# Performance work log

Hardware: AMD Instinct MI355X
Metric: run time of the kernel (lower is better)

The kernel has to match this reference:

```python
import jax, jax.numpy as jnp
import numpy as np

BIT_SHIFT = 8
H, W = 480, 640
N = 100000
C_IN, C_HID, C_OUT = 96, 576, 96


def setup_inputs() -> dict:
    key = jax.random.key(0)
    ks = jax.random.split(key, 12)
    # --- sparse 2D coordinates (unique active sites on an H x W grid) ---
    rng = np.random.default_rng(0)
    lin = rng.choice(H * W, size=N, replace=False)
    ys, xs = lin // W, lin % W
    grid = -np.ones((H, W), dtype=np.int32)
    grid[ys, xs] = np.arange(N, dtype=np.int32)
    # neighbor index for each of the 9 kernel offsets; -1 where no active neighbor
    nbr = np.empty((9, N), dtype=np.int32)
    k = 0
    for dy in (-1, 0, 1):
        for dx in (-1, 0, 1):
            yn, xn = ys + dy, xs + dx
            valid = (yn >= 0) & (yn < H) & (xn >= 0) & (xn < W)
            idx = grid[np.clip(yn, 0, H - 1), np.clip(xn, 0, W - 1)]
            nbr[k] = np.where(valid, idx, -1)
            k += 1
    # --- int8-valued float features / weights (quantized integer inference) ---
    feats = jnp.round(jnp.clip(30.0 * jax.random.normal(ks[0], (N, C_IN)), -127, 127))
    w1 = jnp.round(jnp.clip(40.0 * jax.random.normal(ks[1], (C_IN, C_HID)), -127, 127))
    b1 = jnp.round(1000.0 * jax.random.normal(ks[2], (C_HID,)))
    w2 = jnp.round(jnp.clip(40.0 * jax.random.normal(ks[3], (9, C_HID)), -127, 127))
    b2 = jnp.round(1000.0 * jax.random.normal(ks[4], (C_HID,)))
    w3 = jnp.round(jnp.clip(40.0 * jax.random.normal(ks[5], (C_HID, C_OUT)), -127, 127))
    b3 = jnp.round(1000.0 * jax.random.normal(ks[6], (C_OUT,)))
    # per-output-channel requantization scaling factors (>= ~1 so round() is nonzero)
    s1 = 1.0 + 3.0 * jax.random.uniform(ks[7], (C_HID,))
    s2 = 1.0 + 3.0 * jax.random.uniform(ks[8], (C_HID,))
    s3 = 1.0 + 3.0 * jax.random.uniform(ks[9], (C_OUT,))
    s_main = 1.0 + 2.0 * jax.random.uniform(ks[10], ())
    s_res = 1.0 + 2.0 * jax.random.uniform(ks[11], ())
    return {"feats": feats, "neighbor_idx": jnp.asarray(nbr), "w1": w1, "b1": b1,
            "w2": w2, "b2": b2, "w3": w3, "b3": b3,
            "s1": s1, "s2": s2, "s3": s3, "s_main": s_main, "s_res": s_res}


def _requant(acc, s):
    # fused integer rescale: multiplier m = round(s) * 2^bit_shift, then /2^(2*bit_shift)
    B = 2.0 ** BIT_SHIFT
    return acc * (jnp.round(s) * B) / (B * B)


def _clamp(x):
    lim = 2.0 ** (BIT_SHIFT - 1)
    return jnp.clip(x, -lim, lim)


def _relu6(x):
    return jnp.clip(x, 0.0, 6.0)


def reference(feats, neighbor_idx, w1, b1, w2, b2, w3, b3, s1, s2, s3, s_main, s_res):
    B = 2.0 ** BIT_SHIFT
    # 1x1 expand conv (dense GEMM over active sites)
    x = _relu6(_clamp(_requant(feats @ w1 + b1, s1)))  # [N, C_HID]
    # depthwise 3x3 sparse conv: gather 9 neighbor taps, mask missing sites
    mask = (neighbor_idx >= 0).astype(x.dtype)               # [9, N]
    gathered = x[jnp.clip(neighbor_idx, 0, None)] * mask[:, :, None]  # [9, N, C_HID]
    dw = jnp.einsum('knc,kc->nc', gathered, w2) + b2
    x = _relu6(_clamp(_requant(dw, s2)))
    # 1x1 project conv
    x = _clamp(_requant(x @ w3 + b3, s3))                    # [N, C_OUT]
    # scaled residual add
    out = jnp.round(s_main) * B * x + jnp.round(s_res) * B * feats
    return out
```

## Files before the change

kernel.cpp:

```cpp
#include <hip/hip_runtime.h>
#include <hip/hip_bf16.h>
#include <hip/hip_fp16.h>

#define NS   100000
#define CIN  96
#define CHID 576
#define COUT 96
#define SPB  32
#define LDH  (CHID + 8)
#define CPT  8
#define NG   (CHID / CPT)
#define NSLOT (576 / NG)
#define SPS  (SPB / NSLOT)

typedef float    floatx4 __attribute__((ext_vector_type(4)));
typedef int      intx4   __attribute__((ext_vector_type(4)));
typedef short    short8  __attribute__((ext_vector_type(8)));
typedef _Float16 half8   __attribute__((ext_vector_type(8)));
typedef _Float16 half4   __attribute__((ext_vector_type(4)));

__global__ void prep_kernel(const float* __restrict__ w1, const float* __restrict__ w3,
                            const float* __restrict__ w2,
                            unsigned short* __restrict__ w1T, _Float16* __restrict__ w3T,
                            _Float16* __restrict__ w2h, _Float16* __restrict__ x1h) {
  int i = blockIdx.x * blockDim.x + threadIdx.x;
  if (i >= CHID * CIN) return;
  if (i < CHID) x1h[(size_t)NS * CHID + i] = (_Float16)0.0f;
  if (i < 9 * CHID) w2h[i] = (_Float16)w2[i];
  {
    int h = i / CIN, k = i % CIN;
    w1T[i] = (unsigned short)(__float_as_uint(w1[k * CHID + h]) >> 16);
  }
  {
    int o = i / CHID, k = i % CHID;
    w3T[i] = (_Float16)w3[k * COUT + o];
  }
}

__global__ __launch_bounds__(64) void expand_kernel(
    const float* __restrict__ feats, const float* __restrict__ b1,
    const float* __restrict__ s1, const unsigned short* __restrict__ w1T,
    _Float16* __restrict__ x1h) {
  const int lane = threadIdx.x;
  const int m = lane & 15, quad = lane >> 4;
  const int s0 = blockIdx.x * 64;

  short8 bfrag[4][3];
#pragma unroll
  for (int u = 0; u < 4; ++u) {
    const int site = min(s0 + u * 16 + m, NS - 1);
    const float* frow = feats + (size_t)site * CIN + quad * 8;
#pragma unroll
    for (int kc = 0; kc < 3; ++kc) {
      const float4 lo = *reinterpret_cast<const float4*>(frow + kc * 32);
      const float4 hi = *reinterpret_cast<const float4*>(frow + kc * 32 + 4);
      const float v[8] = {lo.x, lo.y, lo.z, lo.w, hi.x, hi.y, hi.z, hi.w};
#pragma unroll
      for (int j = 0; j < 8; ++j)
        bfrag[u][kc][j] = (short)(__float_as_uint(v[j]) >> 16);
    }
  }

  const int hq = quad * 4;
#pragma unroll 2
  for (int ht = 0; ht < CHID / 16; ++ht) {
    const unsigned short* wrow = w1T + (ht * 16 + m) * CIN + quad * 8;
    short8 a[3];
#pragma unroll
    for (int kc = 0; kc < 3; ++kc)
      a[kc] = *reinterpret_cast<const short8*>(wrow + kc * 32);

    floatx4 acc[4] = {{0.f, 0.f, 0.f, 0.f}, {0.f, 0.f, 0.f, 0.f},
                      {0.f, 0.f, 0.f, 0.f}, {0.f, 0.f, 0.f, 0.f}};
#pragma unroll
    for (int kc = 0; kc < 3; ++kc)
#pragma unroll
      for (int u = 0; u < 4; ++u)
        acc[u] = __builtin_amdgcn_mfma_f32_16x16x32_bf16(a[kc], bfrag[u][kc], acc[u], 0, 0, 0);

    const floatx4 bv = *reinterpret_cast<const floatx4*>(b1 + ht * 16 + hq);
    const floatx4 sv = *reinterpret_cast<const floatx4*>(s1 + ht * 16 + hq);
    floatx4 sc;
#pragma unroll
    for (int j = 0; j < 4; ++j) sc[j] = rintf(sv[j]) * (1.0f / 256.0f);

#pragma unroll
    for (int u = 0; u < 4; ++u) {
      const int site = s0 + u * 16 + m;
      if (site < NS) {
        half4 r;
#pragma unroll
        for (int j = 0; j < 4; ++j) {
          float v = (acc[u][j] + bv[j]) * sc[j];
          r[j] = (_Float16)fminf(fmaxf(v, 0.0f), 6.0f);
        }
        *reinterpret_cast<half4*>(x1h + (size_t)site * CHID + ht * 16 + hq) = r;
      }
    }
  }
}

__global__ __launch_bounds__(576, 8) void dwproj_kernel(
    const int* __restrict__ nbr, const _Float16* __restrict__ w2h,
    const float* __restrict__ b2, const float* __restrict__ s2,
    const _Float16* __restrict__ x1h, const _Float16* __restrict__ w3T,
    const float* __restrict__ feats, const float* __restrict__ b3,
    const float* __restrict__ s3, const float* __restrict__ s_main,
    const float* __restrict__ s_res, float* __restrict__ out) {
  __shared__ _Float16 x2t[SPB * LDH];
  __shared__ int offt[SPB * 12];
  const int t = threadIdx.x;
  const int s0 = blockIdx.x * SPB;

  if (t < SPB * 9) {
    const int k = t >> 5, n = t & 31;
    const int idx = nbr[k * NS + s0 + n];
    offt[n * 12 + k] = (idx < 0 ? NS : idx) * CHID;
  }
  __syncthreads();

  {
    const int g = t % NG;
    const int slot = t / NG;
    const int c0 = g * CPT;
    half8 wv[9];
#pragma unroll
    for (int k = 0; k < 9; ++k)
      wv[k] = *reinterpret_cast<const half8*>(w2h + k * CHID + c0);

#pragma unroll
    for (int i = 0; i < SPS; ++i) {
      const int n = slot * SPS + i;
      const intx4 oa = *reinterpret_cast<const intx4*>(offt + n * 12);
      const intx4 ob = *reinterpret_cast<const intx4*>(offt + n * 12 + 4);
      const int o8 = offt[n * 12 + 8];
      half8 v0 = *reinterpret_cast<const half8*>(x1h + (size_t)oa.x + c0);
      half8 v1 = *reinterpret_cast<const half8*>(x1h + (size_t)oa.y + c0);
      half8 v2 = *reinterpret_cast<const half8*>(x1h + (size_t)oa.z + c0);
      half8 v3 = *reinterpret_cast<const half8*>(x1h + (size_t)oa.w + c0);
      half8 v4 = *reinterpret_cast<const half8*>(x1h + (size_t)ob.x + c0);
      half8 v5 = *reinterpret_cast<const half8*>(x1h + (size_t)ob.y + c0);
      half8 v6 = *reinterpret_cast<const half8*>(x1h + (size_t)ob.z + c0);
      half8 v7 = *reinterpret_cast<const half8*>(x1h + (size_t)ob.w + c0);
      half8 v8 = *reinterpret_cast<const half8*>(x1h + (size_t)o8 + c0);
      float acc[8];
      {
        const floatx4 b0 = *reinterpret_cast<const floatx4*>(b2 + c0);
        const floatx4 b1v = *reinterpret_cast<const floatx4*>(b2 + c0 + 4);
#pragma unroll
        for (int j = 0; j < 4; ++j) { acc[j] = b0[j]; acc[j + 4] = b1v[j]; }
      }
#pragma unroll
      for (int j = 0; j < 8; ++j) {
        acc[j] += (float)v0[j] * (float)wv[0][j];
        acc[j] += (float)v1[j] * (float)wv[1][j];
        acc[j] += (float)v2[j] * (float)wv[2][j];
        acc[j] += (float)v3[j] * (float)wv[3][j];
        acc[j] += (float)v4[j] * (float)wv[4][j];
        acc[j] += (float)v5[j] * (float)wv[5][j];
        acc[j] += (float)v6[j] * (float)wv[6][j];
        acc[j] += (float)v7[j] * (float)wv[7][j];
        acc[j] += (float)v8[j] * (float)wv[8][j];
      }
      const floatx4 sa = *reinterpret_cast<const floatx4*>(s2 + c0);
      const floatx4 sb = *reinterpret_cast<const floatx4*>(s2 + c0 + 4);
      half8 r;
#pragma unroll
      for (int j = 0; j < 4; ++j) {
        float va = acc[j]     * (rintf(sa[j]) * (1.0f / 256.0f));
        float vb = acc[j + 4] * (rintf(sb[j]) * (1.0f / 256.0f));
        r[j]     = (_Float16)fminf(fmaxf(va, 0.0f), 6.0f);
        r[j + 4] = (_Float16)fminf(fmaxf(vb, 0.0f), 6.0f);
      }
      *reinterpret_cast<half8*>(x2t + n * LDH + c0) = r;
    }
  }
  __syncthreads();

  const int wave = t >> 6, lane = t & 63;
  const int m = lane & 15, quad = lane >> 4;
  const float rsm = rintf(s_main[0]) * 256.0f;
  const float rsr = rintf(s_res[0]) * 256.0f;

  for (int tile = wave; tile < (SPB / 16) * (COUT / 16); tile += 9) {
    const int tm = tile / (COUT / 16);
    const int ot = tile % (COUT / 16);
    floatx4 acc = {0.f, 0.f, 0.f, 0.f};
    const _Float16* arow = w3T + (ot * 16 + m) * CHID + quad * 8;
    const _Float16* blds = x2t + (tm * 16 + m) * LDH + quad * 8;
#pragma unroll
    for (int kc = 0; kc < 18; ++kc) {
      const half8 a = *reinterpret_cast<const half8*>(arow + kc * 32);
      const half8 b = *reinterpret_cast<const half8*>(blds + kc * 32);
      acc = __builtin_amdgcn_mfma_f32_16x16x32_f16(a, b, acc, 0, 0, 0);
    }
    const int site = s0 + tm * 16 + m;
    const int o0 = ot * 16 + quad * 4;
    const floatx4 b3v = *reinterpret_cast<const floatx4*>(b3 + o0);
    const floatx4 s3v = *reinterpret_cast<const floatx4*>(s3 + o0);
    const floatx4 fv =
        *reinterpret_cast<const floatx4*>(feats + (size_t)site * COUT + o0);
    floatx4 r;
#pragma unroll
    for (int j = 0; j < 4; ++j) {
      float v = (acc[j] + b3v[j]) * (rintf(s3v[j]) * (1.0f / 256.0f));
      v = fminf(fmaxf(v, -128.0f), 128.0f);
      r[j] = rsm * v + rsr * fv[j];
    }
    *reinterpret_cast<floatx4*>(out + (size_t)site * COUT + o0) = r;
  }
}

extern "C" void kernel_launch(void* const* d_in, const int* in_sizes, int n_in,
                              void* d_out, int out_size, void* d_ws, size_t ws_size,
                              hipStream_t stream) {
  const float* feats  = (const float*)d_in[0];
  const int*   nbr    = (const int*)d_in[1];
  const float* w1     = (const float*)d_in[2];
  const float* b1     = (const float*)d_in[3];
  const float* w2     = (const float*)d_in[4];
  const float* b2     = (const float*)d_in[5];
  const float* w3     = (const float*)d_in[6];
  const float* b3     = (const float*)d_in[7];
  const float* s1     = (const float*)d_in[8];
  const float* s2     = (const float*)d_in[9];
  const float* s3     = (const float*)d_in[10];
  const float* s_main = (const float*)d_in[11];
  const float* s_res  = (const float*)d_in[12];
  float* out = (float*)d_out;

  char* ws = (char*)d_ws;
  _Float16*       x1h = (_Float16*)ws;
  unsigned short* w1T = (unsigned short*)(ws + 115201152);
  _Float16*       w3T = (_Float16*)(ws + 115311744);
  _Float16*       w2h = (_Float16*)(ws + 115422336);

  prep_kernel<<<(CHID * CIN + 255) / 256, 256, 0, stream>>>(w1, w3, w2, w1T, w3T, w2h, x1h);
  expand_kernel<<<(NS + 63) / 64, 64, 0, stream>>>(feats, b1, s1, w1T, x1h);
  dwproj_kernel<<<NS / SPB, 576, 0, stream>>>(nbr, w2h, b2, s2, x1h, w3T,
                                              feats, b3, s3, s_main, s_res, out);
}
```

Measured before the change: 342.9 us.

## Split expand across four waves and shrink dwproj blocks to 256 threads

The expand kernel now launches 256 threads per block, with each of the four waves computing 9 of the 36 hidden-channel tiles for the same 64 sites. This gives four times more waves in flight and less serial work per wave. The dwproj kernel drops from 576 to 256 threads and walks the 32x72 (site, channel-group) work items in 9 strided iterations. Depthwise weights are now reloaded every iteration instead of held in registers, and the projection MFMA tiles are spread over 4 waves instead of 9. The aim is better occupancy and latency hiding, at the cost of redundant feature loads in expand and more serial projection work per wave.

```diff
diff --git a/kernel.cpp b/kernel.cpp
--- a/kernel.cpp
+++ b/kernel.cpp
@@ -8,10 +8,6 @@
 #define COUT 96
 #define SPB  32
 #define LDH  (CHID + 8)
-#define CPT  8
-#define NG   (CHID / CPT)
-#define NSLOT (576 / NG)
-#define SPS  (SPB / NSLOT)
 
 typedef float    floatx4 __attribute__((ext_vector_type(4)));
 typedef int      intx4   __attribute__((ext_vector_type(4)));
@@ -37,11 +33,12 @@
   }
 }
 
-__global__ __launch_bounds__(64) void expand_kernel(
+__global__ __launch_bounds__(256, 4) void expand_kernel(
     const float* __restrict__ feats, const float* __restrict__ b1,
     const float* __restrict__ s1, const unsigned short* __restrict__ w1T,
     _Float16* __restrict__ x1h) {
-  const int lane = threadIdx.x;
+  const int t = threadIdx.x;
+  const int wave = t >> 6, lane = t & 63;
   const int m = lane & 15, quad = lane >> 4;
   const int s0 = blockIdx.x * 64;
 
@@ -62,8 +59,9 @@
   }
 
   const int hq = quad * 4;
-#pragma unroll 2
-  for (int ht = 0; ht < CHID / 16; ++ht) {
+  const int ht0 = wave * 9;
+#pragma unroll 3
+  for (int ht = ht0; ht < ht0 + 9; ++ht) {
     const unsigned short* wrow = w1T + (ht * 16 + m) * CIN + quad * 8;
     short8 a[3];
 #pragma unroll
@@ -100,7 +98,7 @@
   }
 }
 
-__global__ __launch_bounds__(576, 8) void dwproj_kernel(
+__global__ __launch_bounds__(256, 4) void dwproj_kernel(
     const int* __restrict__ nbr, const _Float16* __restrict__ w2h,
     const float* __restrict__ b2, const float* __restrict__ s2,
     const _Float16* __restrict__ x1h, const _Float16* __restrict__ w3T,
@@ -112,68 +110,70 @@
   const int t = threadIdx.x;
   const int s0 = blockIdx.x * SPB;
 
-  if (t < SPB * 9) {
-    const int k = t >> 5, n = t & 31;
+  for (int i = t; i < SPB * 9; i += 256) {
+    const int k = i >> 5, n = i & 31;
     const int idx = nbr[k * NS + s0 + n];
     offt[n * 12 + k] = (idx < 0 ? NS : idx) * CHID;
   }
   __syncthreads();
 
-  {
-    const int g = t % NG;
-    const int slot = t / NG;
-    const int c0 = g * CPT;
-    half8 wv[9];
-#pragma unroll
-    for (int k = 0; k < 9; ++k)
-      wv[k] = *reinterpret_cast<const half8*>(w2h + k * CHID + c0);
-
-#pragma unroll
-    for (int i = 0; i < SPS; ++i) {
-      const int n = slot * SPS + i;
-      const intx4 oa = *reinterpret_cast<const intx4*>(offt + n * 12);
-      const intx4 ob = *reinterpret_cast<const intx4*>(offt + n * 12 + 4);
-      const int o8 = offt[n * 12 + 8];
-      half8 v0 = *reinterpret_cast<const half8*>(x1h + (size_t)oa.x + c0);
-      half8 v1 = *reinterpret_cast<const half8*>(x1h + (size_t)oa.y + c0);
-      half8 v2 = *reinterpret_cast<const half8*>(x1h + (size_t)oa.z + c0);
-      half8 v3 = *reinterpret_cast<const half8*>(x1h + (size_t)oa.w + c0);
-      half8 v4 = *reinterpret_cast<const half8*>(x1h + (size_t)ob.x + c0);
-      half8 v5 = *reinterpret_cast<const half8*>(x1h + (size_t)ob.y + c0);
-      half8 v6 = *reinterpret_cast<const half8*>(x1h + (size_t)ob.z + c0);
-      half8 v7 = *reinterpret_cast<const half8*>(x1h + (size_t)ob.w + c0);
-      half8 v8 = *reinterpret_cast<const half8*>(x1h + (size_t)o8 + c0);
-      float acc[8];
-      {
-        const floatx4 b0 = *reinterpret_cast<const floatx4*>(b2 + c0);
-        const floatx4 b1v = *reinterpret_cast<const floatx4*>(b2 + c0 + 4);
-#pragma unroll
-        for (int j = 0; j < 4; ++j) { acc[j] = b0[j]; acc[j + 4] = b1v[j]; }
-      }
-#pragma unroll
-      for (int j = 0; j < 8; ++j) {
-        acc[j] += (float)v0[j] * (float)wv[0][j];
-        acc[j] += (float)v1[j] * (float)wv[1][j];
-        acc[j] += (float)v2[j] * (float)wv[2][j];
-        acc[j] += (float)v3[j] * (float)wv[3][j];
-        acc[j] += (float)v4[j] * (float)wv[4][j];
-        acc[j] += (float)v5[j] * (float)wv[5][j];
-        acc[j] += (float)v6[j] * (float)wv[6][j];
-        acc[j] += (float)v7[j] * (float)wv[7][j];
-        acc[j] += (float)v8[j] * (float)wv[8][j];
-      }
-      const floatx4 sa = *reinterpret_cast<const floatx4*>(s2 + c0);
-      const floatx4 sb = *reinterpret_cast<const floatx4*>(s2 + c0 + 4);
-      half8 r;
-#pragma unroll
-      for (int j = 0; j < 4; ++j) {
-        float va = acc[j]     * (rintf(sa[j]) * (1.0f / 256.0f));
-        float vb = acc[j + 4] * (rintf(sb[j]) * (1.0f / 256.0f));
-        r[j]     = (_Float16)fminf(fmaxf(va, 0.0f), 6.0f);
-        r[j + 4] = (_Float16)fminf(fmaxf(vb, 0.0f), 6.0f);
-      }
-      *reinterpret_cast<half8*>(x2t + n * LDH + c0) = r;
-    }
+#pragma unroll
+  for (int i = 0; i < 9; ++i) {
+    const int u = i * 256 + t;
+    const int n = u / 72;
+    const int c0 = (u - n * 72) * 8;
+    const int* op = offt + n * 12;
+    const intx4 oa = *reinterpret_cast<const intx4*>(op);
+    const intx4 ob = *reinterpret_cast<const intx4*>(op + 4);
+    const int o8 = op[8];
+    half8 v0 = *reinterpret_cast<const half8*>(x1h + (size_t)oa.x + c0);
+    half8 v1 = *reinterpret_cast<const half8*>(x1h + (size_t)oa.y + c0);
+    half8 v2 = *reinterpret_cast<const half8*>(x1h + (size_t)oa.z + c0);
+    half8 v3 = *reinterpret_cast<const half8*>(x1h + (size_t)oa.w + c0);
+    half8 v4 = *reinterpret_cast<const half8*>(x1h + (size_t)ob.x + c0);
+    half8 v5 = *reinterpret_cast<const half8*>(x1h + (size_t)ob.y + c0);
+    half8 v6 = *reinterpret_cast<const half8*>(x1h + (size_t)ob.z + c0);
+    half8 v7 = *reinterpret_cast<const half8*>(x1h + (size_t)ob.w + c0);
+    half8 v8 = *reinterpret_cast<const half8*>(x1h + (size_t)o8 + c0);
+    half8 w0 = *reinterpret_cast<const half8*>(w2h + 0 * CHID + c0);
+    half8 w1 = *reinterpret_cast<const half8*>(w2h + 1 * CHID + c0);
+    half8 w2v = *reinterpret_cast<const half8*>(w2h + 2 * CHID + c0);
+    half8 w3v = *reinterpret_cast<const half8*>(w2h + 3 * CHID + c0);
+    half8 w4 = *reinterpret_cast<const half8*>(w2h + 4 * CHID + c0);
+    half8 w5 = *reinterpret_cast<const half8*>(w2h + 5 * CHID + c0);
+    half8 w6 = *reinterpret_cast<const half8*>(w2h + 6 * CHID + c0);
+    half8 w7 = *reinterpret_cast<const half8*>(w2h + 7 * CHID + c0);
+    half8 w8 = *reinterpret_cast<const half8*>(w2h + 8 * CHID + c0);
+    float acc[8];
+    {
+      const floatx4 ba = *reinterpret_cast<const floatx4*>(b2 + c0);
+      const floatx4 bb = *reinterpret_cast<const floatx4*>(b2 + c0 + 4);
+#pragma unroll
+      for (int j = 0; j < 4; ++j) { acc[j] = ba[j]; acc[j + 4] = bb[j]; }
+    }
+#pragma unroll
+    for (int j = 0; j < 8; ++j) {
+      acc[j] += (float)v0[j] * (float)w0[j];
+      acc[j] += (float)v1[j] * (float)w1[j];
+      acc[j] += (float)v2[j] * (float)w2v[j];
+      acc[j] += (float)v3[j] * (float)w3v[j];
+      acc[j] += (float)v4[j] * (float)w4[j];
+      acc[j] += (float)v5[j] * (float)w5[j];
+      acc[j] += (float)v6[j] * (float)w6[j];
+      acc[j] += (float)v7[j] * (float)w7[j];
+      acc[j] += (float)v8[j] * (float)w8[j];
+    }
+    const floatx4 sa = *reinterpret_cast<const floatx4*>(s2 + c0);
+    const floatx4 sb = *reinterpret_cast<const floatx4*>(s2 + c0 + 4);
+    half8 r;
+#pragma unroll
+    for (int j = 0; j < 4; ++j) {
+      float va = acc[j]     * (rintf(sa[j]) * (1.0f / 256.0f));
+      float vb = acc[j + 4] * (rintf(sb[j]) * (1.0f / 256.0f));
+      r[j]     = (_Float16)fminf(fmaxf(va, 0.0f), 6.0f);
+      r[j + 4] = (_Float16)fminf(fmaxf(vb, 0.0f), 6.0f);
+    }
+    *reinterpret_cast<half8*>(x2t + n * LDH + c0) = r;
   }
   __syncthreads();
 
@@ -182,7 +182,7 @@
   const float rsm = rintf(s_main[0]) * 256.0f;
   const float rsr = rintf(s_res[0]) * 256.0f;
 
-  for (int tile = wave; tile < (SPB / 16) * (COUT / 16); tile += 9) {
+  for (int tile = wave; tile < (SPB / 16) * (COUT / 16); tile += 4) {
     const int tm = tile / (COUT / 16);
     const int ot = tile % (COUT / 16);
     floatx4 acc = {0.f, 0.f, 0.f, 0.f};
@@ -236,7 +236,7 @@
   _Float16*       w2h = (_Float16*)(ws + 115422336);
 
   prep_kernel<<<(CHID * CIN + 255) / 256, 256, 0, stream>>>(w1, w3, w2, w1T, w3T, w2h, x1h);
-  expand_kernel<<<(NS + 63) / 64, 64, 0, stream>>>(feats, b1, s1, w1T, x1h);
-  dwproj_kernel<<<NS / SPB, 576, 0, stream>>>(nbr, w2h, b2, s2, x1h, w3T,
+  expand_kernel<<<(NS + 63) / 64, 256, 0, stream>>>(feats, b1, s1, w1T, x1h);
+  dwproj_kernel<<<NS / SPB, 256, 0, stream>>>(nbr, w2h, b2, s2, x1h, w3T,
                                               feats, b3, s3, s_main, s_res, out);
 }
```

Measured after the change: 341.0 us. About the same (-0.6%).
